# Performance work log

Measured on AMD Instinct MI355X. Metric: run time of the kernel, lower is better.

Reference implementation:

```python
import jax, jax.numpy as jnp
import numpy as np

B, I, H = 4096, 1024, 1024


def setup_inputs() -> dict:
    key = jax.random.key(0)
    ks = jax.random.split(key, 7)
    s = 0.1  # matches uniform(-0.1, 0.1) init scale loosely
    return {
        "input": jax.random.normal(ks[0], (B, I), jnp.float32),
        "h_t": jax.random.normal(ks[1], (B, H), jnp.float32),
        "c_t": jax.random.normal(ks[2], (B, H), jnp.float32),
        "w_i": jax.random.uniform(ks[3], (I, 4 * H), jnp.float32, -s, s),
        "w_h": jax.random.uniform(ks[4], (H, 4 * H), jnp.float32, -s, s),
        "b_i": jax.random.uniform(ks[5], (4 * H,), jnp.float32, -s, s),
        "b_h": jax.random.uniform(ks[6], (4 * H,), jnp.float32, -s, s),
    }


def reference(input, h_t, c_t, w_i, w_h, b_i, b_h):
    # ifgo: [B, 4H] = x @ w_i + h @ w_h + b_i + b_h
    ifgo = input @ w_i + h_t @ w_h + (b_i + b_h)
    i, f, g, o = jnp.split(ifgo, 4, axis=1)
    i = jax.nn.sigmoid(i)
    f = jax.nn.sigmoid(f)
    g = jnp.tanh(g)
    o = jax.nn.sigmoid(o)
    c_new = f * c_t + i * g
    h_new = o * jnp.tanh(c_new)
    return (h_new, c_new)
```

## Files before the change

kernel.cpp:

```cpp
#include <hip/hip_runtime.h>
#include <stdint.h>

typedef __attribute__((ext_vector_type(8))) short short8;
typedef __attribute__((ext_vector_type(4))) float floatx4;

__device__ inline unsigned short f2bf(float x) {
  union { float f; unsigned int u; } v; v.f = x;
  unsigned int r = v.u + 0x7FFFu + ((v.u >> 16) & 1u);
  return (unsigned short)(r >> 16);
}

__global__ void pack_a(const float* __restrict__ x, const float* __restrict__ h,
                       unsigned short* __restrict__ A) {
  int idx = blockIdx.x * 256 + threadIdx.x;
  int row = idx >> 8;
  int kc  = (idx & 255) << 3;
  const float* src = (kc < 1024) ? (x + (size_t)row * 1024 + kc)
                                 : (h + (size_t)row * 1024 + (kc - 1024));
  float4 a = ((const float4*)src)[0];
  float4 b = ((const float4*)src)[1];
  uint4 o;
  o.x = f2bf(a.x) | ((unsigned)f2bf(a.y) << 16);
  o.y = f2bf(a.z) | ((unsigned)f2bf(a.w) << 16);
  o.z = f2bf(b.x) | ((unsigned)f2bf(b.y) << 16);
  o.w = f2bf(b.z) | ((unsigned)f2bf(b.w) << 16);
  *(uint4*)(A + (size_t)row * 2048 + kc) = o;
}

__global__ void pack_w(const float* __restrict__ wi, const float* __restrict__ wh,
                       unsigned short* __restrict__ Wt) {
  __shared__ float tile[64][65];
  int kt = blockIdx.x & 31;
  int nt = blockIdx.x >> 5;
  int k0 = kt << 6, n0 = nt << 6;
  const float* src = (k0 < 1024) ? (wi + (size_t)k0 * 4096)
                                 : (wh + (size_t)(k0 - 1024) * 4096);
  int t = threadIdx.x;
  int c4 = (t & 15) << 2, rr = t >> 4;
#pragma unroll
  for (int p = 0; p < 4; ++p) {
    int kk = rr + p * 16;
    float4 v = *(const float4*)(src + (size_t)kk * 4096 + n0 + c4);
    tile[kk][c4 + 0] = v.x; tile[kk][c4 + 1] = v.y;
    tile[kk][c4 + 2] = v.z; tile[kk][c4 + 3] = v.w;
  }
  __syncthreads();
  int k8 = (t & 7) << 3, nn = t >> 3;
#pragma unroll
  for (int p = 0; p < 2; ++p) {
    int n = nn + p * 32;
    uint4 o;
    o.x = f2bf(tile[k8 + 0][n]) | ((unsigned)f2bf(tile[k8 + 1][n]) << 16);
    o.y = f2bf(tile[k8 + 2][n]) | ((unsigned)f2bf(tile[k8 + 3][n]) << 16);
    o.z = f2bf(tile[k8 + 4][n]) | ((unsigned)f2bf(tile[k8 + 5][n]) << 16);
    o.w = f2bf(tile[k8 + 6][n]) | ((unsigned)f2bf(tile[k8 + 7][n]) << 16);
    *(uint4*)(Wt + (size_t)(n0 + n) * 2048 + k0 + k8) = o;
  }
}

__device__ inline void gl_lds16(const void* g, void* l) {
  __builtin_amdgcn_global_load_lds(
      (const __attribute__((address_space(1))) void*)g,
      (__attribute__((address_space(3))) void*)l, 16, 0, 0);
}

__device__ inline float sigm(float x)  { return 1.0f / (1.0f + __expf(-x)); }
__device__ inline float tanhx(float x) { return 2.0f / (1.0f + __expf(-2.0f * x)) - 1.0f; }

__global__ void gemm_lstm(const unsigned short* __restrict__ A,
                          const unsigned short* __restrict__ Bt,
                          const float* __restrict__ ct,
                          const float* __restrict__ bi,
                          const float* __restrict__ bh,
                          float* __restrict__ out) {
  constexpr int K = 2048;
  __shared__ char AsB[128 * 64];
  __shared__ char BsB[128 * 64];
  const int tid  = threadIdx.x;
  const int lane = tid & 63;
  const int wave = tid >> 6;
  const int wm = wave >> 1, wn = wave & 1;
  const int m0 = blockIdx.y << 7;
  const int h0 = blockIdx.x << 5;

  const int r  = tid >> 2;
  const int cb = (tid & 3) << 4;
  const char* aS0 = (const char*)A + (size_t)(m0 + r) * K * 2 + cb;
  const char* aS1 = aS0 + (size_t)64 * K * 2;
  const int nB0 = ((r >> 4) & 3) * 1024 + h0 + (r & 15);
  const int nB1 = ((r >> 4) & 3) * 1024 + h0 + 16 + (r & 15);
  const char* bS0 = (const char*)Bt + (size_t)nB0 * K * 2 + cb;
  const char* bS1 = (const char*)Bt + (size_t)nB1 * K * 2 + cb;
  char* aD0 = AsB + tid * 16;
  char* aD1 = AsB + 4096 + tid * 16;
  char* bD0 = BsB + tid * 16;
  char* bD1 = BsB + 4096 + tid * 16;

  floatx4 acc[4][4] = {};
  const int rA = (wm << 6) + (lane & 15);
  const int rB = (wn << 6) + (lane & 15);
  const int kb = (lane >> 4) << 4;

  for (int ks = 0; ks < K; ks += 32) {
    gl_lds16(aS0, aD0); gl_lds16(aS1, aD1);
    gl_lds16(bS0, bD0); gl_lds16(bS1, bD1);
    aS0 += 64; aS1 += 64; bS0 += 64; bS1 += 64;
    __syncthreads();
    short8 af[4], bfr[4];
#pragma unroll
    for (int f = 0; f < 4; ++f) {
      af[f]  = *(const short8*)(AsB + (rA + f * 16) * 64 + kb);
      bfr[f] = *(const short8*)(BsB + (rB + f * 16) * 64 + kb);
    }
#pragma unroll
    for (int i = 0; i < 4; ++i)
#pragma unroll
      for (int j = 0; j < 4; ++j)
        acc[i][j] = __builtin_amdgcn_mfma_f32_16x16x32_bf16(af[i], bfr[j], acc[i][j], 0, 0, 0);
    __syncthreads();
  }

  const int er = (lane >> 4) << 2;
  const int ec = lane & 15;
  const int h  = h0 + (wn << 4) + ec;
  float bias[4];
#pragma unroll
  for (int j = 0; j < 4; ++j) bias[j] = bi[j * 1024 + h] + bh[j * 1024 + h];

#pragma unroll
  for (int i = 0; i < 4; ++i) {
#pragma unroll
    for (int rg = 0; rg < 4; ++rg) {
      int row = m0 + (wm << 6) + i * 16 + er + rg;
      size_t o = (size_t)row * 1024 + h;
      float cv = ct[o];
      float iv = sigm(acc[i][0][rg] + bias[0]);
      float fv = sigm(acc[i][1][rg] + bias[1]);
      float gv = tanhx(acc[i][2][rg] + bias[2]);
      float ov = sigm(acc[i][3][rg] + bias[3]);
      float cn = fv * cv + iv * gv;
      out[o] = ov * tanhx(cn);
      out[4194304 + o] = cn;
    }
  }
}

extern "C" void kernel_launch(void* const* d_in, const int* in_sizes, int n_in,
                              void* d_out, int out_size, void* d_ws, size_t ws_size,
                              hipStream_t stream) {
  const float* x  = (const float*)d_in[0];
  const float* ht = (const float*)d_in[1];
  const float* ct = (const float*)d_in[2];
  const float* wi = (const float*)d_in[3];
  const float* wh = (const float*)d_in[4];
  const float* bi = (const float*)d_in[5];
  const float* bh = (const float*)d_in[6];
  float* out = (float*)d_out;

  char* ws = (char*)d_ws;
  unsigned short* Abf = (unsigned short*)ws;
  unsigned short* Wbf = (unsigned short*)(ws + (16u << 20));

  pack_a<<<4096, 256, 0, stream>>>(x, ht, Abf);
  pack_w<<<2048, 256, 0, stream>>>(wi, wh, Wbf);
  gemm_lstm<<<dim3(32, 32), 256, 0, stream>>>(Abf, Wbf, ct, bi, bh, out);
}
```

Before: 228.0 us.

## Merge pack kernels, pre-permute weight rows for contiguous B loads, prefetch c_t

Combines the activation and weight packing kernels into one launch with a block-index branch, which removes one kernel launch and lets both packing jobs share the GPU. The weight packing now writes rows in a permuted order so each GEMM block reads 128 contiguous rows of B instead of four strided 16-row groups. The bias and c_t loads are also hoisted before the main loop so their latency overlaps the GEMM, at the cost of 16 more live registers per thread, which could lower occupancy.

```diff
diff --git a/kernel.cpp b/kernel.cpp
--- a/kernel.cpp
+++ b/kernel.cpp
@@ -10,51 +10,57 @@
   return (unsigned short)(r >> 16);
 }
 
-__global__ void pack_a(const float* __restrict__ x, const float* __restrict__ h,
-                       unsigned short* __restrict__ A) {
-  int idx = blockIdx.x * 256 + threadIdx.x;
-  int row = idx >> 8;
-  int kc  = (idx & 255) << 3;
-  const float* src = (kc < 1024) ? (x + (size_t)row * 1024 + kc)
-                                 : (h + (size_t)row * 1024 + (kc - 1024));
-  float4 a = ((const float4*)src)[0];
-  float4 b = ((const float4*)src)[1];
-  uint4 o;
-  o.x = f2bf(a.x) | ((unsigned)f2bf(a.y) << 16);
-  o.y = f2bf(a.z) | ((unsigned)f2bf(a.w) << 16);
-  o.z = f2bf(b.x) | ((unsigned)f2bf(b.y) << 16);
-  o.w = f2bf(b.z) | ((unsigned)f2bf(b.w) << 16);
-  *(uint4*)(A + (size_t)row * 2048 + kc) = o;
-}
-
-__global__ void pack_w(const float* __restrict__ wi, const float* __restrict__ wh,
-                       unsigned short* __restrict__ Wt) {
-  __shared__ float tile[64][65];
-  int kt = blockIdx.x & 31;
-  int nt = blockIdx.x >> 5;
-  int k0 = kt << 6, n0 = nt << 6;
-  const float* src = (k0 < 1024) ? (wi + (size_t)k0 * 4096)
-                                 : (wh + (size_t)(k0 - 1024) * 4096);
+__global__ void pack_all(const float* __restrict__ x, const float* __restrict__ h,
+                         const float* __restrict__ wi, const float* __restrict__ wh,
+                         unsigned short* __restrict__ A,
+                         unsigned short* __restrict__ Wt) {
+  int bid = blockIdx.x;
   int t = threadIdx.x;
-  int c4 = (t & 15) << 2, rr = t >> 4;
+  if (bid < 4096) {
+    int idx = bid * 256 + t;
+    int row = idx >> 8;
+    int kc  = (idx & 255) << 3;
+    const float* src = (kc < 1024) ? (x + (size_t)row * 1024 + kc)
+                                   : (h + (size_t)row * 1024 + (kc - 1024));
+    float4 a = ((const float4*)src)[0];
+    float4 b = ((const float4*)src)[1];
+    uint4 o;
+    o.x = f2bf(a.x) | ((unsigned)f2bf(a.y) << 16);
+    o.y = f2bf(a.z) | ((unsigned)f2bf(a.w) << 16);
+    o.z = f2bf(b.x) | ((unsigned)f2bf(b.y) << 16);
+    o.w = f2bf(b.z) | ((unsigned)f2bf(b.w) << 16);
+    *(uint4*)(A + (size_t)row * 2048 + kc) = o;
+  } else {
+    __shared__ float tile[64][65];
+    int b2 = bid - 4096;
+    int kt = b2 & 31;
+    int nt = b2 >> 5;
+    int k0 = kt << 6, n0 = nt << 6;
+    const float* src = (k0 < 1024) ? (wi + (size_t)k0 * 4096)
+                                   : (wh + (size_t)(k0 - 1024) * 4096);
+    int c4 = (t & 15) << 2, rr = t >> 4;
 #pragma unroll
-  for (int p = 0; p < 4; ++p) {
-    int kk = rr + p * 16;
-    float4 v = *(const float4*)(src + (size_t)kk * 4096 + n0 + c4);
-    tile[kk][c4 + 0] = v.x; tile[kk][c4 + 1] = v.y;
-    tile[kk][c4 + 2] = v.z; tile[kk][c4 + 3] = v.w;
-  }
-  __syncthreads();
-  int k8 = (t & 7) << 3, nn = t >> 3;
+    for (int p = 0; p < 4; ++p) {
+      int kk = rr + p * 16;
+      float4 v = *(const float4*)(src + (size_t)kk * 4096 + n0 + c4);
+      tile[kk][c4 + 0] = v.x; tile[kk][c4 + 1] = v.y;
+      tile[kk][c4 + 2] = v.z; tile[kk][c4 + 3] = v.w;
+    }
+    __syncthreads();
+    int k8 = (t & 7) << 3, nn = t >> 3;
 #pragma unroll
-  for (int p = 0; p < 2; ++p) {
-    int n = nn + p * 32;
-    uint4 o;
-    o.x = f2bf(tile[k8 + 0][n]) | ((unsigned)f2bf(tile[k8 + 1][n]) << 16);
-    o.y = f2bf(tile[k8 + 2][n]) | ((unsigned)f2bf(tile[k8 + 3][n]) << 16);
-    o.z = f2bf(tile[k8 + 4][n]) | ((unsigned)f2bf(tile[k8 + 5][n]) << 16);
-    o.w = f2bf(tile[k8 + 6][n]) | ((unsigned)f2bf(tile[k8 + 7][n]) << 16);
-    *(uint4*)(Wt + (size_t)(n0 + n) * 2048 + k0 + k8) = o;
+    for (int p = 0; p < 2; ++p) {
+      int n = n0 + nn + p * 32;
+      int hh = n & 1023, g = n >> 10;
+      int R = ((hh >> 5) << 7) + (((hh >> 4) & 1) << 6) + (g << 4) + (hh & 15);
+      int nl = nn + p * 32;
+      uint4 o;
+      o.x = f2bf(tile[k8 + 0][nl]) | ((unsigned)f2bf(tile[k8 + 1][nl]) << 16);
+      o.y = f2bf(tile[k8 + 2][nl]) | ((unsigned)f2bf(tile[k8 + 3][nl]) << 16);
+      o.z = f2bf(tile[k8 + 4][nl]) | ((unsigned)f2bf(tile[k8 + 5][nl]) << 16);
+      o.w = f2bf(tile[k8 + 6][nl]) | ((unsigned)f2bf(tile[k8 + 7][nl]) << 16);
+      *(uint4*)(Wt + (size_t)R * 2048 + k0 + k8) = o;
+    }
   }
 }
 
@@ -81,16 +87,30 @@
   const int wave = tid >> 6;
   const int wm = wave >> 1, wn = wave & 1;
   const int m0 = blockIdx.y << 7;
+  const int n0 = blockIdx.x << 7;
   const int h0 = blockIdx.x << 5;
+
+  const int er = (lane >> 4) << 2;
+  const int ec = lane & 15;
+  const int h  = h0 + (wn << 4) + ec;
+  float bias[4];
+#pragma unroll
+  for (int j = 0; j < 4; ++j) bias[j] = bi[j * 1024 + h] + bh[j * 1024 + h];
+  float cpre[4][4];
+#pragma unroll
+  for (int i = 0; i < 4; ++i)
+#pragma unroll
+    for (int rg = 0; rg < 4; ++rg) {
+      int row = m0 + (wm << 6) + i * 16 + er + rg;
+      cpre[i][rg] = ct[(size_t)row * 1024 + h];
+    }
 
   const int r  = tid >> 2;
   const int cb = (tid & 3) << 4;
   const char* aS0 = (const char*)A + (size_t)(m0 + r) * K * 2 + cb;
   const char* aS1 = aS0 + (size_t)64 * K * 2;
-  const int nB0 = ((r >> 4) & 3) * 1024 + h0 + (r & 15);
-  const int nB1 = ((r >> 4) & 3) * 1024 + h0 + 16 + (r & 15);
-  const char* bS0 = (const char*)Bt + (size_t)nB0 * K * 2 + cb;
-  const char* bS1 = (const char*)Bt + (size_t)nB1 * K * 2 + cb;
+  const char* bS0 = (const char*)Bt + (size_t)(n0 + r) * K * 2 + cb;
+  const char* bS1 = bS0 + (size_t)64 * K * 2;
   char* aD0 = AsB + tid * 16;
   char* aD1 = AsB + 4096 + tid * 16;
   char* bD0 = BsB + tid * 16;
@@ -120,25 +140,17 @@
     __syncthreads();
   }
 
-  const int er = (lane >> 4) << 2;
-  const int ec = lane & 15;
-  const int h  = h0 + (wn << 4) + ec;
-  float bias[4];
-#pragma unroll
-  for (int j = 0; j < 4; ++j) bias[j] = bi[j * 1024 + h] + bh[j * 1024 + h];
-
 #pragma unroll
   for (int i = 0; i < 4; ++i) {
 #pragma unroll
     for (int rg = 0; rg < 4; ++rg) {
       int row = m0 + (wm << 6) + i * 16 + er + rg;
       size_t o = (size_t)row * 1024 + h;
-      float cv = ct[o];
       float iv = sigm(acc[i][0][rg] + bias[0]);
       float fv = sigm(acc[i][1][rg] + bias[1]);
       float gv = tanhx(acc[i][2][rg] + bias[2]);
       float ov = sigm(acc[i][3][rg] + bias[3]);
-      float cn = fv * cv + iv * gv;
+      float cn = fv * cpre[i][rg] + iv * gv;
       out[o] = ov * tanhx(cn);
       out[4194304 + o] = cn;
     }
@@ -161,7 +173,6 @@
   unsigned short* Abf = (unsigned short*)ws;
   unsigned short* Wbf = (unsigned short*)(ws + (16u << 20));
 
-  pack_a<<<4096, 256, 0, stream>>>(x, ht, Abf);
-  pack_w<<<2048, 256, 0, stream>>>(wi, wh, Wbf);
+  pack_all<<<6144, 256, 0, stream>>>(x, ht, wi, wh, Abf, Wbf);
   gemm_lstm<<<dim3(32, 32), 256, 0, stream>>>(Abf, Wbf, ct, bi, bh, out);
 }
```

After: 225.2 us. Within noise of the previous version (-1.3%).
